# Kernel tuning notes

Measured on AMD Instinct MI355X. Metric: run time of the kernel, lower is better.

The kernel has to match this reference:

```python
import jax, jax.numpy as jnp
import numpy as np

B, S, F = 32, 576, 700          # batch, nodes (24*24), features per node
D, K = 16, 1024                 # latent/embedding dim, codebook size
ENC = [512, 256]
DEC = [1024, 512]


def _dense_init(key, fan_in, fan_out):
    kw, kb = jax.random.split(key)
    w = jax.random.normal(kw, (fan_in, fan_out), dtype=jnp.float32) * (1.0 / np.sqrt(fan_in))
    b = jnp.zeros((fan_out,), dtype=jnp.float32)
    return w, b


def setup_inputs() -> dict:
    key = jax.random.key(0)
    ks = jax.random.split(key, 10)
    x = jax.random.uniform(ks[0], (B, S, F), dtype=jnp.float32)
    eps = jax.random.normal(ks[1], (B, S, D), dtype=jnp.float32)
    ew0, eb0 = _dense_init(ks[2], F, ENC[0])
    ew1, eb1 = _dense_init(ks[3], ENC[0], ENC[1])
    ew2, eb2 = _dense_init(ks[4], ENC[1], 2 * D)
    dw0, db0 = _dense_init(ks[5], S * D, DEC[0])
    dw1, db1 = _dense_init(ks[6], DEC[0], DEC[1])
    dw2, db2 = _dense_init(ks[7], DEC[1], S * F)
    codebook = jax.random.uniform(ks[8], (K, D), minval=-0.05, maxval=0.05, dtype=jnp.float32)
    return {"x": x, "eps": eps,
            "ew0": ew0, "eb0": eb0, "ew1": ew1, "eb1": eb1, "ew2": ew2, "eb2": eb2,
            "dw0": dw0, "db0": db0, "dw1": dw1, "db1": db1, "dw2": dw2, "db2": db2,
            "codebook": codebook}


def reference(x, eps, ew0, eb0, ew1, eb1, ew2, eb2,
              dw0, db0, dw1, db1, dw2, db2, codebook):
    # --- encoder (TimeDistributed Dense over nodes) ---
    h = jax.nn.relu(x @ ew0 + eb0)
    h = jax.nn.relu(h @ ew1 + eb1)
    enc = h @ ew2 + eb2                      # [B, S, 2D]
    mean, log_var = jnp.split(enc, 2, axis=-1)
    # --- reparameterize ---
    z_e = mean + jnp.exp(0.5 * log_var) * eps  # [B, S, D]
    # --- vector quantization: squared L2 distances, argmin, gather ---
    # ||z - c||^2 = ||z||^2 - 2 z.c + ||c||^2  (same math as broadcast sum)
    z_sq = jnp.sum(z_e * z_e, axis=-1, keepdims=True)          # [B, S, 1]
    c_sq = jnp.sum(codebook * codebook, axis=-1)               # [K]
    distances = z_sq - 2.0 * jnp.einsum('bsd,kd->bsk', z_e, codebook) + c_sq  # [B,S,K]
    encoding_indices = jnp.argmin(distances, axis=-1)          # [B, S]
    z_q = codebook[encoding_indices]                           # [B, S, D]
    # straight-through estimator
    z_q_st = z_e + jax.lax.stop_gradient(z_q - z_e)
    # --- decoder (flattened input) ---
    zf = z_q_st.reshape(z_q_st.shape[0], -1)                   # [B, S*D]
    h = jax.nn.relu(zf @ dw0 + db0)
    h = jax.nn.relu(h @ dw1 + db1)
    reconstructed = jax.nn.softplus(h @ dw2 + db2).reshape(-1, S, F)
    vq_loss = jnp.mean(jnp.square(jax.lax.stop_gradient(z_e) - z_q))
    return reconstructed, mean, log_var, vq_loss
```

## Files before the change

### kernel.cpp

```cpp
#include <hip/hip_runtime.h>
#include <math.h>

#define B_  32
#define S_  576
#define F_  700
#define D_  16
#define KC  1024
#define M_  (B_*S_)
#define SD  (S_*D_)
#define SF  (S_*F_)

#define OFF_H0   0ull
#define OFF_H1   9437184ull
#define OFF_ZE   14155776ull
#define OFF_ZQT  14450688ull
#define OFF_HD0  14745600ull
#define OFF_HD1T 14778368ull
#define OFF_LOSS 14794752ull
#define OFF_WT   14794816ull
#define WT_EH0   0ull
#define WT_EL0   360448ull
#define WT_EH1   720896ull
#define WT_EL1   851968ull

#define OUT_MEAN 12902400
#define OUT_LV   13197312
#define OUT_LOSS 13492224

typedef __attribute__((ext_vector_type(8))) short short8;
typedef __attribute__((ext_vector_type(4))) short short4v;
typedef __attribute__((ext_vector_type(4))) float floatx4;

__device__ __forceinline__ unsigned short f2bf(float f) {
  unsigned u = __float_as_uint(f);
  return (unsigned short)((u + 0x7FFFu + ((u >> 16) & 1u)) >> 16);
}
__device__ __forceinline__ float bf2f(unsigned short h) {
  return __uint_as_float((unsigned)h << 16);
}

__global__ void wprep(const float* __restrict__ W, unsigned short* __restrict__ WhT,
                      unsigned short* __restrict__ WlT, int K, int N, int Kpad) {
  __shared__ float t[32][33];
  const int n0 = blockIdx.x * 32, k0 = blockIdx.y * 32;
  const int tx = threadIdx.x & 31, ty = threadIdx.x >> 5;
  #pragma unroll
  for (int i = 0; i < 4; ++i) {
    int k = k0 + ty + i * 8;
    t[ty + i * 8][tx] = (k < K) ? W[(size_t)k * N + n0 + tx] : 0.f;
  }
  __syncthreads();
  #pragma unroll
  for (int i = 0; i < 4; ++i) {
    int n = ty + i * 8;
    float v = t[tx][n];
    unsigned short h = f2bf(v);
    unsigned short l = f2bf(v - bf2f(h));
    size_t o = (size_t)(n0 + n) * Kpad + k0 + tx;
    WhT[o] = h;
    WlT[o] = l;
  }
}

__global__ __launch_bounds__(256) void mfma_gemm_relu(
    const float* __restrict__ A, const unsigned short* __restrict__ WhT,
    const unsigned short* __restrict__ WlT, const float* __restrict__ bias,
    float* __restrict__ C, int N, int K, int nkt) {
  __shared__ unsigned short Ah[128][40], Al[128][40];
  __shared__ unsigned short Bh[128][40], Bl[128][40];
  const int tid = threadIdx.x;
  const int n0 = blockIdx.x * 128, m0 = blockIdx.y * 128;
  const int srow = tid >> 3;
  const int skk  = (tid & 7) << 2;
  const int wid = tid >> 6, lane = tid & 63;
  const int q = lane >> 4, r16 = lane & 15;
  const int wm = (wid & 1) << 6, wn = (wid >> 1) << 6;
  const int Kp = nkt << 5;
  floatx4 acc[4][4] = {};

  for (int kt = 0; kt < nkt; ++kt) {
    const int k0 = kt << 5;
    #pragma unroll
    for (int p = 0; p < 4; ++p) {
      const int row = p * 32 + srow;
      float4 v = make_float4(0.f, 0.f, 0.f, 0.f);
      if (k0 + skk < K)
        v = *(const float4*)(A + (size_t)(m0 + row) * K + k0 + skk);
      unsigned short hx = f2bf(v.x), hy = f2bf(v.y), hz = f2bf(v.z), hw = f2bf(v.w);
      short4v hv = { (short)hx, (short)hy, (short)hz, (short)hw };
      short4v lv = { (short)f2bf(v.x - bf2f(hx)), (short)f2bf(v.y - bf2f(hy)),
                     (short)f2bf(v.z - bf2f(hz)), (short)f2bf(v.w - bf2f(hw)) };
      *(short4v*)&Ah[row][skk] = hv;
      *(short4v*)&Al[row][skk] = lv;
      size_t bo = (size_t)(n0 + row) * Kp + k0 + skk;
      *(short4v*)&Bh[row][skk] = *(const short4v*)(WhT + bo);
      *(short4v*)&Bl[row][skk] = *(const short4v*)(WlT + bo);
    }
    __syncthreads();
    short8 ah[4], al[4];
    #pragma unroll
    for (int mi = 0; mi < 4; ++mi) {
      ah[mi] = *(const short8*)&Ah[wm + mi * 16 + r16][q * 8];
      al[mi] = *(const short8*)&Al[wm + mi * 16 + r16][q * 8];
    }
    #pragma unroll
    for (int ni = 0; ni < 4; ++ni) {
      short8 bh = *(const short8*)&Bh[wn + ni * 16 + r16][q * 8];
      short8 bl = *(const short8*)&Bl[wn + ni * 16 + r16][q * 8];
      #pragma unroll
      for (int mi = 0; mi < 4; ++mi) {
        acc[mi][ni] = __builtin_amdgcn_mfma_f32_16x16x32_bf16(ah[mi], bh, acc[mi][ni], 0, 0, 0);
        acc[mi][ni] = __builtin_amdgcn_mfma_f32_16x16x32_bf16(ah[mi], bl, acc[mi][ni], 0, 0, 0);
        acc[mi][ni] = __builtin_amdgcn_mfma_f32_16x16x32_bf16(al[mi], bh, acc[mi][ni], 0, 0, 0);
      }
    }
    __syncthreads();
  }
  #pragma unroll
  for (int ni = 0; ni < 4; ++ni) {
    const int col = n0 + wn + ni * 16 + r16;
    const float bv = bias[col];
    #pragma unroll
    for (int mi = 0; mi < 4; ++mi) {
      const int row = m0 + wm + mi * 16 + q * 4;
      #pragma unroll
      for (int rg = 0; rg < 4; ++rg) {
        float val = acc[mi][ni][rg] + bv;
        C[(size_t)(row + rg) * N + col] = fmaxf(val, 0.f);
      }
    }
  }
}

__global__ __launch_bounds__(256) void enc2_reparam(
    const float* __restrict__ h1, const float* __restrict__ ew2,
    const float* __restrict__ eb2, const float* __restrict__ eps,
    float* __restrict__ mean_out, float* __restrict__ lv_out,
    float* __restrict__ z_e) {
  __shared__ float hs[8][256];
  __shared__ float es[8][32];
  const int tid = threadIdx.x;
  const int r0 = blockIdx.x * 8;
  {
    int lr = tid >> 5, lc = (tid & 31) << 3;
    const float* src = h1 + (size_t)(r0 + lr) * 256 + lc;
    *(float4*)&hs[lr][lc]   = *(const float4*)src;
    *(float4*)&hs[lr][lc+4] = *(const float4*)(src + 4);
  }
  __syncthreads();
  const int r = tid >> 5, c = tid & 31;
  float sum = eb2[c];
  #pragma unroll 8
  for (int k = 0; k < 256; ++k)
    sum = fmaf(hs[r][k], ew2[k*32 + c], sum);
  es[r][c] = sum;
  __syncthreads();
  if (c < 16) {
    int row = r0 + r;
    float m  = es[r][c];
    float lv = es[r][c+16];
    mean_out[(size_t)row*16 + c] = m;
    lv_out[(size_t)row*16 + c]   = lv;
    z_e[(size_t)row*16 + c] = fmaf(expf(0.5f*lv), eps[(size_t)row*16 + c], m);
  }
}

__global__ __launch_bounds__(256) void vq_kernel(
    const float* __restrict__ z_e, const float* __restrict__ cb,
    float* __restrict__ zqT, float* __restrict__ loss_acc) {
  __shared__ float red_d[256];
  __shared__ int   red_i[256];
  const int tid = threadIdx.x;
  const int lane = tid & 63;
  const int wave = tid >> 6;
  const int row = blockIdx.x * 64 + lane;

  float z[16];
  {
    const float4* zp = (const float4*)(z_e + (size_t)row * 16);
    *(float4*)&z[0]  = zp[0];
    *(float4*)&z[4]  = zp[1];
    *(float4*)&z[8]  = zp[2];
    *(float4*)&z[12] = zp[3];
  }

  float dmin = 1e30f;
  int   imin = 0;
  const float4* cp = ((const float4*)cb) + (size_t)wave * 256 * 4;
  #pragma unroll 4
  for (int j = 0; j < 256; ++j) {
    float4 c0 = cp[0], c1 = cp[1], c2 = cp[2], c3 = cp[3];
    cp += 4;
    float d = 0.f, t;
    t = z[0]-c0.x;  d = fmaf(t,t,d);  t = z[1]-c0.y;  d = fmaf(t,t,d);
    t = z[2]-c0.z;  d = fmaf(t,t,d);  t = z[3]-c0.w;  d = fmaf(t,t,d);
    t = z[4]-c1.x;  d = fmaf(t,t,d);  t = z[5]-c1.y;  d = fmaf(t,t,d);
    t = z[6]-c1.z;  d = fmaf(t,t,d);  t = z[7]-c1.w;  d = fmaf(t,t,d);
    t = z[8]-c2.x;  d = fmaf(t,t,d);  t = z[9]-c2.y;  d = fmaf(t,t,d);
    t = z[10]-c2.z; d = fmaf(t,t,d);  t = z[11]-c2.w; d = fmaf(t,t,d);
    t = z[12]-c3.x; d = fmaf(t,t,d);  t = z[13]-c3.y; d = fmaf(t,t,d);
    t = z[14]-c3.z; d = fmaf(t,t,d);  t = z[15]-c3.w; d = fmaf(t,t,d);
    int c = wave * 256 + j;
    if (d < dmin) { dmin = d; imin = c; }
  }
  red_d[tid] = dmin;
  red_i[tid] = imin;
  __syncthreads();
  if (tid < 64) {
    #pragma unroll
    for (int w = 1; w < 4; ++w) {
      float d2 = red_d[w*64 + lane];
      int   i2 = red_i[w*64 + lane];
      if (d2 < dmin || (d2 == dmin && i2 < imin)) { dmin = d2; imin = i2; }
    }
    float ssum = 0.f;
    int b = row / S_, s = row - b * S_;
    float* zt = zqT + (size_t)s * 16 * 32 + b;
    const float* cq = cb + (size_t)imin * 16;
    #pragma unroll
    for (int e = 0; e < 16; ++e) {
      float qv = cq[e];
      float diff = z[e] - qv;
      ssum = fmaf(diff, diff, ssum);
      zt[e * 32] = qv;
    }
    #pragma unroll
    for (int off = 32; off > 0; off >>= 1)
      ssum += __shfl_down(ssum, off, 64);
    if (lane == 0) atomicAdd(loss_acc, ssum);
  }
}

__global__ __launch_bounds__(256) void dec0_kernel(
    const float* __restrict__ zqT, const float* __restrict__ dw0,
    float* __restrict__ hd0_pre) {
  __shared__ float At[256 * 32];
  const int tid = threadIdx.x;
  const int n  = blockIdx.x * 256 + tid;
  const int k0 = blockIdx.y * 256;
  {
    const float4* src = (const float4*)(zqT + (size_t)k0 * 32);
    float4* dst = (float4*)At;
    #pragma unroll
    for (int i = 0; i < 8; ++i) dst[tid + 256*i] = src[tid + 256*i];
  }
  __syncthreads();
  float acc[32] = {};
  const float* wp = dw0 + (size_t)k0 * 1024 + n;
  #pragma unroll 2
  for (int k = 0; k < 256; ++k) {
    float w = wp[(size_t)k * 1024];
    const float4* ap = (const float4*)&At[k * 32];
    #pragma unroll
    for (int mm = 0; mm < 8; ++mm) {
      float4 a = ap[mm];
      acc[mm*4+0] = fmaf(a.x, w, acc[mm*4+0]);
      acc[mm*4+1] = fmaf(a.y, w, acc[mm*4+1]);
      acc[mm*4+2] = fmaf(a.z, w, acc[mm*4+2]);
      acc[mm*4+3] = fmaf(a.w, w, acc[mm*4+3]);
    }
  }
  #pragma unroll
  for (int m = 0; m < 32; ++m)
    atomicAdd(&hd0_pre[m*1024 + n], acc[m]);
}

__global__ __launch_bounds__(256) void dec1_kernel(
    const float* __restrict__ hd0_pre, const float* __restrict__ db0,
    const float* __restrict__ dw1, const float* __restrict__ db1,
    float* __restrict__ hd1T) {
  __shared__ float As[1024];
  const int tid = threadIdx.x;
  const int m = blockIdx.x;
  for (int i = tid; i < 1024; i += 256)
    As[i] = fmaxf(hd0_pre[m*1024 + i] + db0[i], 0.f);
  __syncthreads();
  const int n = blockIdx.y * 256 + tid;
  float acc = db1[n];
  #pragma unroll 4
  for (int k = 0; k < 1024; ++k)
    acc = fmaf(As[k], dw1[(size_t)k * 512 + n], acc);
  hd1T[n*32 + m] = fmaxf(acc, 0.f);
}

__global__ __launch_bounds__(256) void dec2_kernel(
    const float* __restrict__ hd1T, const float* __restrict__ dw2,
    const float* __restrict__ db2, float* __restrict__ out) {
  __shared__ float At[512 * 32];
  const int tid = threadIdx.x;
  {
    const float4* src = (const float4*)hd1T;
    float4* dst = (float4*)At;
    #pragma unroll
    for (int i = 0; i < 16; ++i) dst[tid + 256*i] = src[tid + 256*i];
  }
  __syncthreads();
  const int n = blockIdx.x * 512 + tid * 2;
  if (n >= SF) return;
  float2 acc[32];
  #pragma unroll
  for (int m = 0; m < 32; ++m) { acc[m].x = 0.f; acc[m].y = 0.f; }
  const float* wp = dw2 + n;
  #pragma unroll 2
  for (int k = 0; k < 512; ++k) {
    float2 w = *(const float2*)(wp + (size_t)k * SF);
    const float4* ap = (const float4*)&At[k * 32];
    #pragma unroll
    for (int mm = 0; mm < 8; ++mm) {
      float4 a = ap[mm];
      acc[mm*4+0].x = fmaf(a.x, w.x, acc[mm*4+0].x);
      acc[mm*4+0].y = fmaf(a.x, w.y, acc[mm*4+0].y);
      acc[mm*4+1].x = fmaf(a.y, w.x, acc[mm*4+1].x);
      acc[mm*4+1].y = fmaf(a.y, w.y, acc[mm*4+1].y);
      acc[mm*4+2].x = fmaf(a.z, w.x, acc[mm*4+2].x);
      acc[mm*4+2].y = fmaf(a.z, w.y, acc[mm*4+2].y);
      acc[mm*4+3].x = fmaf(a.w, w.x, acc[mm*4+3].x);
      acc[mm*4+3].y = fmaf(a.w, w.y, acc[mm*4+3].y);
    }
  }
  float2 bb = *(const float2*)(db2 + n);
  #pragma unroll
  for (int m = 0; m < 32; ++m) {
    float x0 = acc[m].x + bb.x;
    float x1 = acc[m].y + bb.y;
    float2 o;
    o.x = fmaxf(x0, 0.f) + log1pf(expf(-fabsf(x0)));
    o.y = fmaxf(x1, 0.f) + log1pf(expf(-fabsf(x1)));
    *(float2*)(out + (size_t)m * SF + n) = o;
  }
}

__global__ void finalize_loss(const float* __restrict__ loss_acc,
                              float* __restrict__ out_loss) {
  *out_loss = *loss_acc * (1.f / 294912.f);
}

extern "C" void kernel_launch(void* const* d_in, const int* in_sizes, int n_in,
                              void* d_out, int out_size, void* d_ws, size_t ws_size,
                              hipStream_t stream) {
  const float* x   = (const float*)d_in[0];
  const float* eps = (const float*)d_in[1];
  const float* ew0 = (const float*)d_in[2];
  const float* eb0 = (const float*)d_in[3];
  const float* ew1 = (const float*)d_in[4];
  const float* eb1 = (const float*)d_in[5];
  const float* ew2 = (const float*)d_in[6];
  const float* eb2 = (const float*)d_in[7];
  const float* dw0 = (const float*)d_in[8];
  const float* db0 = (const float*)d_in[9];
  const float* dw1 = (const float*)d_in[10];
  const float* db1 = (const float*)d_in[11];
  const float* dw2 = (const float*)d_in[12];
  const float* db2 = (const float*)d_in[13];
  const float* cbk = (const float*)d_in[14];
  float* out = (float*)d_out;
  float* ws  = (float*)d_ws;

  float* h0   = ws + OFF_H0;
  float* h1   = ws + OFF_H1;
  float* ze   = ws + OFF_ZE;
  float* zqT  = ws + OFF_ZQT;
  float* hd0  = ws + OFF_HD0;
  float* hd1T = ws + OFF_HD1T;
  float* lac  = ws + OFF_LOSS;
  unsigned short* wt = (unsigned short*)(ws + OFF_WT);
  unsigned short* ewh0T = wt + WT_EH0;
  unsigned short* ewl0T = wt + WT_EL0;
  unsigned short* ewh1T = wt + WT_EH1;
  unsigned short* ewl1T = wt + WT_EL1;

  hipMemsetAsync(hd0, 0, 32768 * sizeof(float), stream);
  hipMemsetAsync(lac, 0, sizeof(float), stream);

  wprep<<<dim3(16, 22), 256, 0, stream>>>(ew0, ewh0T, ewl0T, 700, 512, 704);
  wprep<<<dim3(8, 16), 256, 0, stream>>>(ew1, ewh1T, ewl1T, 512, 256, 512);

  mfma_gemm_relu<<<dim3(4, 144), 256, 0, stream>>>(x,  ewh0T, ewl0T, eb0, h0, 512, 700, 22);
  mfma_gemm_relu<<<dim3(2, 144), 256, 0, stream>>>(h0, ewh1T, ewl1T, eb1, h1, 256, 512, 16);

  enc2_reparam<<<2304, 256, 0, stream>>>(h1, ew2, eb2, eps,
                                         out + OUT_MEAN, out + OUT_LV, ze);
  vq_kernel<<<288, 256, 0, stream>>>(ze, cbk, zqT, lac);
  dec0_kernel<<<dim3(4, 36), 256, 0, stream>>>(zqT, dw0, hd0);
  dec1_kernel<<<dim3(32, 2), 256, 0, stream>>>(hd0, db0, dw1, db1, hd1T);
  dec2_kernel<<<788, 256, 0, stream>>>(hd1T, dw2, db2, out);
  finalize_loss<<<1, 1, 0, stream>>>(lac, out + OUT_LOSS);
}
```

Baseline: 1.707 ms.

## Increase parallelism across decoder and VQ kernels with split-K atomics and prefetching

The decoder and VQ stages get more blocks. VQ now handles 32 rows per block, splitting the codebook eight ways. dec0 halves its K chunk and writes a transposed output. dec1 becomes a split-K GEMM with atomics, and dec2 moves to one column per thread, so the db1 bias and ReLU now happen in dec2's smem load. Weight loads in dec0 and dec2 are register double-buffered in groups of eight, and enc2 stages ew2 in shared memory. The changes target under-occupancy of the small decoder GEMMs, at the cost of more atomics and some extra shared-memory traffic. The VQ tie-break on equal distances also changes.

```diff
diff --git a/kernel.cpp b/kernel.cpp
--- a/kernel.cpp
+++ b/kernel.cpp
@@ -137,10 +137,17 @@
     const float* __restrict__ eb2, const float* __restrict__ eps,
     float* __restrict__ mean_out, float* __restrict__ lv_out,
     float* __restrict__ z_e) {
+  __shared__ float ws_[256 * 32];
   __shared__ float hs[8][256];
   __shared__ float es[8][32];
   const int tid = threadIdx.x;
   const int r0 = blockIdx.x * 8;
+  {
+    const float4* src = (const float4*)ew2;
+    float4* dst = (float4*)ws_;
+    #pragma unroll
+    for (int i = 0; i < 8; ++i) dst[tid + 256 * i] = src[tid + 256 * i];
+  }
   {
     int lr = tid >> 5, lc = (tid & 31) << 3;
     const float* src = h1 + (size_t)(r0 + lr) * 256 + lc;
@@ -152,7 +159,7 @@
   float sum = eb2[c];
   #pragma unroll 8
   for (int k = 0; k < 256; ++k)
-    sum = fmaf(hs[r][k], ew2[k*32 + c], sum);
+    sum = fmaf(hs[r][k], ws_[k * 32 + c], sum);
   es[r][c] = sum;
   __syncthreads();
   if (c < 16) {
@@ -171,9 +178,9 @@
   __shared__ float red_d[256];
   __shared__ int   red_i[256];
   const int tid = threadIdx.x;
-  const int lane = tid & 63;
-  const int wave = tid >> 6;
-  const int row = blockIdx.x * 64 + lane;
+  const int r = tid & 31;
+  const int g = tid >> 5;
+  const int row = blockIdx.x * 32 + r;
 
   float z[16];
   {
@@ -185,10 +192,10 @@
   }
 
   float dmin = 1e30f;
-  int   imin = 0;
-  const float4* cp = ((const float4*)cb) + (size_t)wave * 256 * 4;
+  int   imin = g * 128;
+  const float4* cp = ((const float4*)cb) + (size_t)g * 128 * 4;
   #pragma unroll 4
-  for (int j = 0; j < 256; ++j) {
+  for (int j = 0; j < 128; ++j) {
     float4 c0 = cp[0], c1 = cp[1], c2 = cp[2], c3 = cp[3];
     cp += 4;
     float d = 0.f, t;
@@ -200,18 +207,18 @@
     t = z[10]-c2.z; d = fmaf(t,t,d);  t = z[11]-c2.w; d = fmaf(t,t,d);
     t = z[12]-c3.x; d = fmaf(t,t,d);  t = z[13]-c3.y; d = fmaf(t,t,d);
     t = z[14]-c3.z; d = fmaf(t,t,d);  t = z[15]-c3.w; d = fmaf(t,t,d);
-    int c = wave * 256 + j;
+    int c = g * 128 + j;
     if (d < dmin) { dmin = d; imin = c; }
   }
   red_d[tid] = dmin;
   red_i[tid] = imin;
   __syncthreads();
-  if (tid < 64) {
-    #pragma unroll
-    for (int w = 1; w < 4; ++w) {
-      float d2 = red_d[w*64 + lane];
-      int   i2 = red_i[w*64 + lane];
-      if (d2 < dmin || (d2 == dmin && i2 < imin)) { dmin = d2; imin = i2; }
+  if (tid < 32) {
+    #pragma unroll
+    for (int w = 1; w < 8; ++w) {
+      float d2 = red_d[w*32 + tid];
+      int   i2 = red_i[w*32 + tid];
+      if (d2 < dmin) { dmin = d2; imin = i2; }
     }
     float ssum = 0.f;
     int b = row / S_, s = row - b * S_;
@@ -225,108 +232,147 @@
       zt[e * 32] = qv;
     }
     #pragma unroll
-    for (int off = 32; off > 0; off >>= 1)
+    for (int off = 16; off > 0; off >>= 1)
       ssum += __shfl_down(ssum, off, 64);
-    if (lane == 0) atomicAdd(loss_acc, ssum);
+    if (tid == 0) atomicAdd(loss_acc, ssum);
   }
 }
 
 __global__ __launch_bounds__(256) void dec0_kernel(
     const float* __restrict__ zqT, const float* __restrict__ dw0,
-    float* __restrict__ hd0_pre) {
-  __shared__ float At[256 * 32];
+    float* __restrict__ hd0T_pre) {
+  __shared__ float At[128 * 32];
   const int tid = threadIdx.x;
   const int n  = blockIdx.x * 256 + tid;
-  const int k0 = blockIdx.y * 256;
+  const int k0 = blockIdx.y * 128;
   {
     const float4* src = (const float4*)(zqT + (size_t)k0 * 32);
     float4* dst = (float4*)At;
     #pragma unroll
-    for (int i = 0; i < 8; ++i) dst[tid + 256*i] = src[tid + 256*i];
+    for (int i = 0; i < 4; ++i) dst[tid + 256*i] = src[tid + 256*i];
   }
   __syncthreads();
   float acc[32] = {};
   const float* wp = dw0 + (size_t)k0 * 1024 + n;
-  #pragma unroll 2
-  for (int k = 0; k < 256; ++k) {
-    float w = wp[(size_t)k * 1024];
-    const float4* ap = (const float4*)&At[k * 32];
-    #pragma unroll
-    for (int mm = 0; mm < 8; ++mm) {
-      float4 a = ap[mm];
-      acc[mm*4+0] = fmaf(a.x, w, acc[mm*4+0]);
-      acc[mm*4+1] = fmaf(a.y, w, acc[mm*4+1]);
-      acc[mm*4+2] = fmaf(a.z, w, acc[mm*4+2]);
-      acc[mm*4+3] = fmaf(a.w, w, acc[mm*4+3]);
+  float w[8];
+  #pragma unroll
+  for (int j = 0; j < 8; ++j) w[j] = wp[(size_t)j * 1024];
+  for (int kq = 0; kq < 128; kq += 8) {
+    float nw[8];
+    const bool more = (kq + 8) < 128;
+    if (more) {
+      #pragma unroll
+      for (int j = 0; j < 8; ++j) nw[j] = wp[(size_t)(kq + 8 + j) * 1024];
+    }
+    #pragma unroll
+    for (int j = 0; j < 8; ++j) {
+      const float4* ap = (const float4*)&At[(kq + j) * 32];
+      #pragma unroll
+      for (int mm = 0; mm < 8; ++mm) {
+        float4 a = ap[mm];
+        acc[mm*4+0] = fmaf(a.x, w[j], acc[mm*4+0]);
+        acc[mm*4+1] = fmaf(a.y, w[j], acc[mm*4+1]);
+        acc[mm*4+2] = fmaf(a.z, w[j], acc[mm*4+2]);
+        acc[mm*4+3] = fmaf(a.w, w[j], acc[mm*4+3]);
+      }
+    }
+    if (more) {
+      #pragma unroll
+      for (int j = 0; j < 8; ++j) w[j] = nw[j];
     }
   }
   #pragma unroll
   for (int m = 0; m < 32; ++m)
-    atomicAdd(&hd0_pre[m*1024 + n], acc[m]);
+    atomicAdd(&hd0T_pre[(size_t)n * 32 + m], acc[m]);
 }
 
 __global__ __launch_bounds__(256) void dec1_kernel(
-    const float* __restrict__ hd0_pre, const float* __restrict__ db0,
-    const float* __restrict__ dw1, const float* __restrict__ db1,
-    float* __restrict__ hd1T) {
-  __shared__ float As[1024];
-  const int tid = threadIdx.x;
-  const int m = blockIdx.x;
-  for (int i = tid; i < 1024; i += 256)
-    As[i] = fmaxf(hd0_pre[m*1024 + i] + db0[i], 0.f);
-  __syncthreads();
-  const int n = blockIdx.y * 256 + tid;
-  float acc = db1[n];
+    const float* __restrict__ hd0T_pre, const float* __restrict__ db0,
+    const float* __restrict__ dw1, float* __restrict__ hd1T_pre) {
+  __shared__ float As[64 * 32];
+  const int tid = threadIdx.x;
+  const int n0 = blockIdx.x * 32, k0 = blockIdx.y * 64;
+  #pragma unroll
+  for (int i = 0; i < 2; ++i) {
+    int idx4 = tid + 256 * i;
+    int kk = idx4 >> 3;
+    float4 v = ((const float4*)hd0T_pre)[k0 * 8 + idx4];
+    float b = db0[k0 + kk];
+    float4 o = { fmaxf(v.x + b, 0.f), fmaxf(v.y + b, 0.f),
+                 fmaxf(v.z + b, 0.f), fmaxf(v.w + b, 0.f) };
+    ((float4*)As)[idx4] = o;
+  }
+  __syncthreads();
+  const int n = n0 + (tid & 31);
+  const int mg = (tid >> 5) << 2;
+  float acc[4] = {};
+  const float* wp = dw1 + (size_t)k0 * 512 + n;
   #pragma unroll 4
-  for (int k = 0; k < 1024; ++k)
-    acc = fmaf(As[k], dw1[(size_t)k * 512 + n], acc);
-  hd1T[n*32 + m] = fmaxf(acc, 0.f);
+  for (int kk = 0; kk < 64; ++kk) {
+    float w = wp[(size_t)kk * 512];
+    float4 a = *(const float4*)&As[kk * 32 + mg];
+    acc[0] = fmaf(a.x, w, acc[0]);
+    acc[1] = fmaf(a.y, w, acc[1]);
+    acc[2] = fmaf(a.z, w, acc[2]);
+    acc[3] = fmaf(a.w, w, acc[3]);
+  }
+  #pragma unroll
+  for (int j = 0; j < 4; ++j)
+    atomicAdd(&hd1T_pre[(size_t)n * 32 + mg + j], acc[j]);
 }
 
 __global__ __launch_bounds__(256) void dec2_kernel(
-    const float* __restrict__ hd1T, const float* __restrict__ dw2,
-    const float* __restrict__ db2, float* __restrict__ out) {
+    const float* __restrict__ hd1T_pre, const float* __restrict__ db1,
+    const float* __restrict__ dw2, const float* __restrict__ db2,
+    float* __restrict__ out) {
   __shared__ float At[512 * 32];
   const int tid = threadIdx.x;
-  {
-    const float4* src = (const float4*)hd1T;
-    float4* dst = (float4*)At;
-    #pragma unroll
-    for (int i = 0; i < 16; ++i) dst[tid + 256*i] = src[tid + 256*i];
-  }
-  __syncthreads();
-  const int n = blockIdx.x * 512 + tid * 2;
-  if (n >= SF) return;
-  float2 acc[32];
-  #pragma unroll
-  for (int m = 0; m < 32; ++m) { acc[m].x = 0.f; acc[m].y = 0.f; }
+  #pragma unroll
+  for (int i = 0; i < 16; ++i) {
+    int idx4 = tid + 256 * i;
+    int k = idx4 >> 3;
+    float4 v = ((const float4*)hd1T_pre)[idx4];
+    float b = db1[k];
+    float4 o = { fmaxf(v.x + b, 0.f), fmaxf(v.y + b, 0.f),
+                 fmaxf(v.z + b, 0.f), fmaxf(v.w + b, 0.f) };
+    ((float4*)At)[idx4] = o;
+  }
+  __syncthreads();
+  const int n = blockIdx.x * 256 + tid;
+  float acc[32] = {};
   const float* wp = dw2 + n;
-  #pragma unroll 2
-  for (int k = 0; k < 512; ++k) {
-    float2 w = *(const float2*)(wp + (size_t)k * SF);
-    const float4* ap = (const float4*)&At[k * 32];
-    #pragma unroll
-    for (int mm = 0; mm < 8; ++mm) {
-      float4 a = ap[mm];
-      acc[mm*4+0].x = fmaf(a.x, w.x, acc[mm*4+0].x);
-      acc[mm*4+0].y = fmaf(a.x, w.y, acc[mm*4+0].y);
-      acc[mm*4+1].x = fmaf(a.y, w.x, acc[mm*4+1].x);
-      acc[mm*4+1].y = fmaf(a.y, w.y, acc[mm*4+1].y);
-      acc[mm*4+2].x = fmaf(a.z, w.x, acc[mm*4+2].x);
-      acc[mm*4+2].y = fmaf(a.z, w.y, acc[mm*4+2].y);
-      acc[mm*4+3].x = fmaf(a.w, w.x, acc[mm*4+3].x);
-      acc[mm*4+3].y = fmaf(a.w, w.y, acc[mm*4+3].y);
-    }
-  }
-  float2 bb = *(const float2*)(db2 + n);
+  float w[8];
+  #pragma unroll
+  for (int j = 0; j < 8; ++j) w[j] = wp[(size_t)j * SF];
+  for (int k0 = 0; k0 < 512; k0 += 8) {
+    float nw[8];
+    const bool more = (k0 + 8) < 512;
+    if (more) {
+      #pragma unroll
+      for (int j = 0; j < 8; ++j) nw[j] = wp[(size_t)(k0 + 8 + j) * SF];
+    }
+    #pragma unroll
+    for (int j = 0; j < 8; ++j) {
+      const float4* ap = (const float4*)&At[(k0 + j) * 32];
+      #pragma unroll
+      for (int mm = 0; mm < 8; ++mm) {
+        float4 a = ap[mm];
+        acc[mm*4+0] = fmaf(a.x, w[j], acc[mm*4+0]);
+        acc[mm*4+1] = fmaf(a.y, w[j], acc[mm*4+1]);
+        acc[mm*4+2] = fmaf(a.z, w[j], acc[mm*4+2]);
+        acc[mm*4+3] = fmaf(a.w, w[j], acc[mm*4+3]);
+      }
+    }
+    if (more) {
+      #pragma unroll
+      for (int j = 0; j < 8; ++j) w[j] = nw[j];
+    }
+  }
+  const float bb = db2[n];
   #pragma unroll
   for (int m = 0; m < 32; ++m) {
-    float x0 = acc[m].x + bb.x;
-    float x1 = acc[m].y + bb.y;
-    float2 o;
-    o.x = fmaxf(x0, 0.f) + log1pf(expf(-fabsf(x0)));
-    o.y = fmaxf(x1, 0.f) + log1pf(expf(-fabsf(x1)));
-    *(float2*)(out + (size_t)m * SF + n) = o;
+    float xv = acc[m] + bb;
+    out[(size_t)m * SF + n] = fmaxf(xv, 0.f) + log1pf(expf(-fabsf(xv)));
   }
 }
 
@@ -356,21 +402,20 @@
   float* out = (float*)d_out;
   float* ws  = (float*)d_ws;
 
-  float* h0   = ws + OFF_H0;
-  float* h1   = ws + OFF_H1;
-  float* ze   = ws + OFF_ZE;
-  float* zqT  = ws + OFF_ZQT;
-  float* hd0  = ws + OFF_HD0;
-  float* hd1T = ws + OFF_HD1T;
-  float* lac  = ws + OFF_LOSS;
+  float* h0    = ws + OFF_H0;
+  float* h1    = ws + OFF_H1;
+  float* ze    = ws + OFF_ZE;
+  float* zqT   = ws + OFF_ZQT;
+  float* hd0T  = ws + OFF_HD0;
+  float* hd1T  = ws + OFF_HD1T;
+  float* lac   = ws + OFF_LOSS;
   unsigned short* wt = (unsigned short*)(ws + OFF_WT);
   unsigned short* ewh0T = wt + WT_EH0;
   unsigned short* ewl0T = wt + WT_EL0;
   unsigned short* ewh1T = wt + WT_EH1;
   unsigned short* ewl1T = wt + WT_EL1;
 
-  hipMemsetAsync(hd0, 0, 32768 * sizeof(float), stream);
-  hipMemsetAsync(lac, 0, sizeof(float), stream);
+  hipMemsetAsync(hd0T, 0, (32768 + 16384 + 64) * sizeof(float), stream);
 
   wprep<<<dim3(16, 22), 256, 0, stream>>>(ew0, ewh0T, ewl0T, 700, 512, 704);
   wprep<<<dim3(8, 16), 256, 0, stream>>>(ew1, ewh1T, ewl1T, 512, 256, 512);
@@ -380,9 +425,9 @@
 
   enc2_reparam<<<2304, 256, 0, stream>>>(h1, ew2, eb2, eps,
                                          out + OUT_MEAN, out + OUT_LV, ze);
-  vq_kernel<<<288, 256, 0, stream>>>(ze, cbk, zqT, lac);
-  dec0_kernel<<<dim3(4, 36), 256, 0, stream>>>(zqT, dw0, hd0);
-  dec1_kernel<<<dim3(32, 2), 256, 0, stream>>>(hd0, db0, dw1, db1, hd1T);
-  dec2_kernel<<<788, 256, 0, stream>>>(hd1T, dw2, db2, out);
+  vq_kernel<<<576, 256, 0, stream>>>(ze, cbk, zqT, lac);
+  dec0_kernel<<<dim3(4, 72), 256, 0, stream>>>(zqT, dw0, hd0T);
+  dec1_kernel<<<dim3(16, 16), 256, 0, stream>>>(hd0T, db0, dw1, hd1T);
+  dec2_kernel<<<1575, 256, 0, stream>>>(hd1T, db1, dw2, db2, out);
   finalize_loss<<<1, 1, 0, stream>>>(lac, out + OUT_LOSS);
 }
```

Result: faster. 1.665 ms (-2.5%).
